# Kernel tuning notes

Hardware: AMD Instinct MI355X
Metric: run time of the kernel (lower is better)

## Reference

```python
import jax, jax.numpy as jnp
import numpy as np

NEG_SLOPE = 0.2   # PyG GATConv default negative_slope
LN_EPS = 1e-5
SOFTMAX_EPS = 1e-16  # PyG softmax denominator eps


def setup_inputs() -> dict:
    key = jax.random.key(0)
    ks = jax.random.split(key, 6)
    N, IN, OUT, H, E = 100000, 128, 64, 2, 1600000
    X = jax.random.normal(ks[0], (N, IN), dtype=jnp.float32)
    edge_index = jax.random.randint(ks[1], (2, E), 0, N, dtype=jnp.int64)
    W = jax.random.normal(ks[2], (H * OUT, IN), dtype=jnp.float32) * 0.05
    att_src = jax.random.normal(ks[3], (H, OUT), dtype=jnp.float32) * 0.05
    att_dst = jax.random.normal(ks[4], (H, OUT), dtype=jnp.float32) * 0.05
    bias = jnp.zeros((OUT,), dtype=jnp.float32)
    ln_gamma = jnp.ones((OUT,), dtype=jnp.float32)
    ln_beta = jnp.zeros((OUT,), dtype=jnp.float32)
    return {"X": X, "edge_index": edge_index, "W": W, "att_src": att_src,
            "att_dst": att_dst, "bias": bias, "ln_gamma": ln_gamma, "ln_beta": ln_beta}


def reference(X, edge_index, W, att_src, att_dst, bias, ln_gamma, ln_beta):
    N = X.shape[0]
    H, F = att_src.shape
    # PyG GATConv default: add self-loops
    loops = jnp.arange(N, dtype=edge_index.dtype)
    src = jnp.concatenate([edge_index[0], loops])  # [Et]
    dst = jnp.concatenate([edge_index[1], loops])  # [Et]
    # linear projection: x' = X @ W^T  -> [N, H, F]
    x = (X @ W.T).reshape(N, H, F)
    # per-node attention logits  [N, H]
    a_src = jnp.einsum('nhf,hf->nh', x, att_src)
    a_dst = jnp.einsum('nhf,hf->nh', x, att_dst)
    # per-edge logits, leaky relu  [Et, H]
    e = jax.nn.leaky_relu(a_src[src] + a_dst[dst], NEG_SLOPE)
    # segment softmax over incoming edges of each dst node
    m = jax.ops.segment_max(e, dst, num_segments=N)          # [N, H]
    ex = jnp.exp(e - m[dst])
    denom = jax.ops.segment_sum(ex, dst, num_segments=N)     # [N, H]
    alpha = ex / (denom[dst] + SOFTMAX_EPS)                  # [Et, H]
    # weighted scatter-add of source features
    msg = x[src] * alpha[:, :, None]                         # [Et, H, F]
    out = jax.ops.segment_sum(msg, dst, num_segments=N)      # [N, H, F]
    # concat=False -> mean over heads, then bias
    out = out.mean(axis=1) + bias                            # [N, F]
    # LayerNorm over features
    mu = out.mean(axis=-1, keepdims=True)
    var = ((out - mu) ** 2).mean(axis=-1, keepdims=True)
    h = (out - mu) * jax.lax.rsqrt(var + LN_EPS) * ln_gamma + ln_beta
    return h
```

## Files before the change

kernel.cpp:

```cpp
#include <hip/hip_runtime.h>
#include <hip/hip_bf16.h>

#define NEG_SLOPE 0.2f
#define LN_EPS 1e-5f
#define SM_EPS 1e-16f

typedef __attribute__((ext_vector_type(8))) short bf16x8;
typedef __attribute__((ext_vector_type(4))) float f32x4;

__device__ inline unsigned short f2bf(float f) {
    unsigned u = __float_as_uint(f);
    return (unsigned short)((u + 0x7FFFu + ((u >> 16) & 1u)) >> 16);
}
__device__ inline float bf_lo(unsigned int v) { return __uint_as_float(v << 16); }
__device__ inline float bf_hi(unsigned int v) { return __uint_as_float(v & 0xffff0000u); }

#define NBIN 512
#define BCAP 4864
#define SCHUNK 4096
#define CURPAD 16

__global__ __launch_bounds__(256) void k_gemm(const float* __restrict__ X,
                                              const float* __restrict__ W,
                                              const float* __restrict__ att_src,
                                              const float* __restrict__ att_dst,
                                              unsigned int* __restrict__ xp,
                                              float2* __restrict__ aS,
                                              float2* __restrict__ aD,
                                              int* __restrict__ binCursor, int N) {
    __shared__ unsigned short Ws[128 * 136];
    __shared__ unsigned short Xs[64 * 136];
    const int t = threadIdx.x;
    const int b0 = blockIdx.x * 64;
    const int lane = t & 63;
    const int w = t >> 6;
    const int c15 = lane & 15;
    const int quad = lane >> 4;

    if (blockIdx.x == 0) {
        for (int i = t; i < NBIN; i += 256) binCursor[i * CURPAD] = i * BCAP;
    }

#pragma unroll
    for (int i = 0; i < 16; ++i) {
        int f = i * 256 + t;
        int nr = f >> 5;
        int q = f & 31;
        float4 v = reinterpret_cast<const float4*>(W)[nr * 32 + q];
        ushort4 b;
        b.x = f2bf(v.x); b.y = f2bf(v.y); b.z = f2bf(v.z); b.w = f2bf(v.w);
        *reinterpret_cast<ushort4*>(&Ws[nr * 136 + q * 4]) = b;
    }
#pragma unroll
    for (int i = 0; i < 8; ++i) {
        int f = i * 256 + t;
        int m = f >> 5;
        int q = f & 31;
        int gr = b0 + m;
        if (gr >= N) gr = N - 1;
        float4 v = reinterpret_cast<const float4*>(X)[(size_t)gr * 32 + q];
        ushort4 b;
        b.x = f2bf(v.x); b.y = f2bf(v.y); b.z = f2bf(v.z); b.w = f2bf(v.w);
        *reinterpret_cast<ushort4*>(&Xs[m * 136 + q * 4]) = b;
    }
    __syncthreads();

    f32x4 acc[8];
#pragma unroll
    for (int ct = 0; ct < 8; ++ct) acc[ct] = (f32x4){0.f, 0.f, 0.f, 0.f};

#pragma unroll
    for (int kc = 0; kc < 4; ++kc) {
        bf16x8 af = *reinterpret_cast<const bf16x8*>(
            &Xs[(w * 16 + c15) * 136 + kc * 32 + quad * 8]);
#pragma unroll
        for (int ct = 0; ct < 8; ++ct) {
            bf16x8 bfr = *reinterpret_cast<const bf16x8*>(
                &Ws[(ct * 16 + c15) * 136 + kc * 32 + quad * 8]);
            acc[ct] = __builtin_amdgcn_mfma_f32_16x16x32_bf16(af, bfr, acc[ct], 0, 0, 0);
        }
    }

    float attS[8], attD[8];
#pragma unroll
    for (int ct = 0; ct < 8; ++ct) {
        attS[ct] = att_src[ct * 16 + c15];
        attD[ct] = att_dst[ct * 16 + c15];
    }

#pragma unroll
    for (int r = 0; r < 4; ++r) {
        int row = b0 + w * 16 + quad * 4 + r;
        float s0 = 0.f, s1 = 0.f, d0 = 0.f, d1 = 0.f;
#pragma unroll
        for (int ct = 0; ct < 4; ++ct) {
            s0 += acc[ct][r] * attS[ct];
            d0 += acc[ct][r] * attD[ct];
            s1 += acc[ct + 4][r] * attS[ct + 4];
            d1 += acc[ct + 4][r] * attD[ct + 4];
        }
#pragma unroll
        for (int o = 1; o < 16; o <<= 1) {
            s0 += __shfl_xor(s0, o);
            s1 += __shfl_xor(s1, o);
            d0 += __shfl_xor(d0, o);
            d1 += __shfl_xor(d1, o);
        }
        if (row < N) {
#pragma unroll
            for (int ct = 0; ct < 4; ++ct) {
                unsigned int p = (unsigned int)f2bf(acc[ct][r]) |
                                 ((unsigned int)f2bf(acc[ct + 4][r]) << 16);
                xp[(size_t)row * 64 + ct * 16 + c15] = p;
            }
            if (c15 == 0) {
                aS[row] = make_float2(s0, s1);
                aD[row] = make_float2(d0, d1);
            }
        }
    }
}

__global__ __launch_bounds__(256) void k_scatter(const int* __restrict__ ei,
                                                 int* __restrict__ binCursor,
                                                 unsigned int* __restrict__ tmp,
                                                 int E) {
    __shared__ int off[NBIN];
    const int t = threadIdx.x;
    const int base = blockIdx.x * SCHUNK;

    int bn[16];
    unsigned int pe[16];
#pragma unroll
    for (int k = 0; k < 16; ++k) {
        int i = base + k * 256 + t;
        if (i < E) {
            int s = ei[i];
            int d = ei[E + i];
            bn[k] = d >> 8;
            pe[k] = ((unsigned)(d & 255) << 24) | (unsigned)s;
        } else {
            bn[k] = -1;
        }
    }

    for (int i = t; i < NBIN; i += 256) off[i] = 0;
    __syncthreads();
#pragma unroll
    for (int k = 0; k < 16; ++k)
        if (bn[k] >= 0) atomicAdd(&off[bn[k]], 1);
    __syncthreads();
    for (int i = t; i < NBIN; i += 256) {
        int h = off[i];
        off[i] = h ? atomicAdd(&binCursor[i * CURPAD], h) : 0;
    }
    __syncthreads();
#pragma unroll
    for (int k = 0; k < 16; ++k) {
        if (bn[k] >= 0) {
            int p = atomicAdd(&off[bn[k]], 1);
            tmp[p] = pe[k];
        }
    }
}

__global__ __launch_bounds__(512) void k_bucket(const unsigned int* __restrict__ tmp,
                                                const int* __restrict__ binCursor,
                                                unsigned int* __restrict__ csr,
                                                unsigned int* __restrict__ rowPtr,
                                                int N) {
    __shared__ int cnt[256];
    __shared__ int cur[256];
    __shared__ int lds[4];
    const int t = threadIdx.x;
    const int b = blockIdx.x;
    const int start = b * BCAP;
    int m = binCursor[b * CURPAD] - start;
    if (m > BCAP) m = BCAP;

    if (t < 256) cnt[t] = 0;
    __syncthreads();

    for (int k = t; k < m; k += 512) {
        atomicAdd(&cnt[tmp[start + k] >> 24], 1);
    }
    __syncthreads();

    const int lane = t & 63, w = t >> 6;
    int v = 0, incl = 0;
    if (t < 256) {
        v = cnt[t];
        incl = v;
#pragma unroll
        for (int o = 1; o < 64; o <<= 1) {
            int u = __shfl_up(incl, o);
            if (lane >= o) incl += u;
        }
        if (lane == 63) lds[w] = incl;
    }
    __syncthreads();
    if (t == 0) {
        int run = 0;
        for (int i = 0; i < 4; ++i) { int tv = lds[i]; lds[i] = run; run += tv; }
    }
    __syncthreads();
    if (t < 256) {
        int excl = lds[w] + incl - v;
        cur[t] = excl;
        int d = b * 256 + t;
        if (d < N) rowPtr[d] = (unsigned)(start + excl) | ((unsigned)v << 22);
    }
    __syncthreads();

    for (int k = t; k < m; k += 512) {
        unsigned int e = tmp[start + k];
        int p = atomicAdd(&cur[e >> 24], 1);
        csr[start + p] = e & 0x00FFFFFFu;
    }
}

__global__ __launch_bounds__(256) void k_agg(const unsigned int* __restrict__ xp,
                                             const float2* __restrict__ aS,
                                             const float2* __restrict__ aD,
                                             const unsigned int* __restrict__ rowPtr,
                                             const unsigned int* __restrict__ csr,
                                             const float* __restrict__ bias,
                                             const float* __restrict__ gamma,
                                             const float* __restrict__ beta,
                                             float* __restrict__ out, int N) {
    const int w = threadIdx.x >> 6, lane = threadIdx.x & 63;
    const int n = blockIdx.x * 4 + w;
    if (n >= N) return;

    float2 a = aS[n];
    float2 ad2 = aD[n];
    float f0 = a.x + ad2.x; f0 = fmaxf(f0, NEG_SLOPE * f0);
    float f1 = a.y + ad2.y; f1 = fmaxf(f1, NEG_SLOPE * f1);
    float us0 = __expf(f0), us1 = __expf(f1);

    unsigned int vself = xp[((unsigned)n << 6) | lane];
    float S0 = us0 * bf_lo(vself);
    float S1 = us1 * bf_hi(vself);
    float D0 = us0, D1 = us1;

    unsigned int pr = rowPtr[n];
    const int jb = (int)(pr & 0x3FFFFFu);
    const int je = jb + (int)(pr >> 22);
    int j = jb;
    const int nfull = (je - jb) >> 3;

    unsigned int cc[8];
    if (nfull > 0) {
        int ju = __builtin_amdgcn_readfirstlane(j);
#pragma unroll
        for (int q = 0; q < 8; ++q) cc[q] = csr[ju + q];
    }
    for (int bI = 0; bI < nfull; ++bI) {
        unsigned int v[8];
        float2 as_[8];
#pragma unroll
        for (int q = 0; q < 8; ++q) v[q] = xp[(cc[q] << 6) | lane];
#pragma unroll
        for (int q = 0; q < 8; ++q) as_[q] = aS[cc[q]];
        unsigned int cn[8];
        {
            int jn = (bI + 1 < nfull) ? (j + 8) : jb;
            int ju = __builtin_amdgcn_readfirstlane(jn);
#pragma unroll
            for (int q = 0; q < 8; ++q) cn[q] = csr[ju + q];
        }
#pragma unroll
        for (int q = 0; q < 8; ++q) {
            float g0 = as_[q].x + ad2.x; g0 = fmaxf(g0, NEG_SLOPE * g0);
            float g1 = as_[q].y + ad2.y; g1 = fmaxf(g1, NEG_SLOPE * g1);
            float u0 = __expf(g0), u1 = __expf(g1);
            D0 += u0; D1 += u1;
            S0 += u0 * bf_lo(v[q]);
            S1 += u1 * bf_hi(v[q]);
        }
#pragma unroll
        for (int q = 0; q < 8; ++q) cc[q] = cn[q];
        j += 8;
    }
    for (; j + 3 < je; j += 4) {
        int ju = __builtin_amdgcn_readfirstlane(j);
        unsigned int c[4];
#pragma unroll
        for (int q = 0; q < 4; ++q) c[q] = csr[ju + q];
        unsigned int v[4];
        float2 as_[4];
#pragma unroll
        for (int q = 0; q < 4; ++q) v[q] = xp[(c[q] << 6) | lane];
#pragma unroll
        for (int q = 0; q < 4; ++q) as_[q] = aS[c[q]];
#pragma unroll
        for (int q = 0; q < 4; ++q) {
            float g0 = as_[q].x + ad2.x; g0 = fmaxf(g0, NEG_SLOPE * g0);
            float g1 = as_[q].y + ad2.y; g1 = fmaxf(g1, NEG_SLOPE * g1);
            float u0 = __expf(g0), u1 = __expf(g1);
            D0 += u0; D1 += u1;
            S0 += u0 * bf_lo(v[q]);
            S1 += u1 * bf_hi(v[q]);
        }
    }
    for (; j < je; ++j) {
        unsigned int c = csr[__builtin_amdgcn_readfirstlane(j)];
        unsigned int vv = xp[(c << 6) | lane];
        float2 asv = aS[c];
        float g0 = asv.x + ad2.x; g0 = fmaxf(g0, NEG_SLOPE * g0);
        float g1 = asv.y + ad2.y; g1 = fmaxf(g1, NEG_SLOPE * g1);
        float u0 = __expf(g0), u1 = __expf(g1);
        D0 += u0; D1 += u1;
        S0 += u0 * bf_lo(vv);
        S1 += u1 * bf_hi(vv);
    }

    float o = (0.5f / (D0 + SM_EPS)) * S0 + (0.5f / (D1 + SM_EPS)) * S1 + bias[lane];

    float mu = o;
#pragma unroll
    for (int d = 32; d > 0; d >>= 1) mu += __shfl_xor(mu, d);
    mu *= (1.0f / 64.0f);
    float dv = o - mu;
    float var = dv * dv;
#pragma unroll
    for (int d = 32; d > 0; d >>= 1) var += __shfl_xor(var, d);
    var *= (1.0f / 64.0f);
    out[(size_t)n * 64 + lane] = dv * rsqrtf(var + LN_EPS) * gamma[lane] + beta[lane];
}

extern "C" void kernel_launch(void* const* d_in, const int* in_sizes, int n_in,
                              void* d_out, int out_size, void* d_ws, size_t ws_size,
                              hipStream_t stream) {
    const float* X        = (const float*)d_in[0];
    const int*   ei       = (const int*)d_in[1];
    const float* W        = (const float*)d_in[2];
    const float* att_src  = (const float*)d_in[3];
    const float* att_dst  = (const float*)d_in[4];
    const float* bias     = (const float*)d_in[5];
    const float* ln_gamma = (const float*)d_in[6];
    const float* ln_beta  = (const float*)d_in[7];
    float* out = (float*)d_out;

    const int N = in_sizes[0] / 128;
    const int E = in_sizes[1] / 2;
    const int NBUCK = (N + 255) / 256;

    char* ws = (char*)d_ws;
    size_t off = 0;
    auto alloc = [&](size_t bytes) {
        size_t o = off;
        off += (bytes + 255) & ~(size_t)255;
        return o;
    };
    unsigned int* xp     = (unsigned int*)(ws + alloc((size_t)N * 64 * 4));
    float2* aS           = (float2*)(ws + alloc((size_t)N * 8));
    float2* aD           = (float2*)(ws + alloc((size_t)N * 8));
    unsigned int* rowPtr = (unsigned int*)(ws + alloc((size_t)N * 4));
    unsigned int* csr    = (unsigned int*)(ws + alloc((size_t)NBIN * BCAP * 4));
    unsigned int* tmp    = (unsigned int*)(ws + alloc((size_t)NBIN * BCAP * 4));
    int* binCursor       = (int*)(ws + alloc(NBIN * CURPAD * 4));

    k_gemm<<<(N + 63) / 64, 256, 0, stream>>>(X, W, att_src, att_dst, xp, aS, aD,
                                              binCursor, N);
    k_scatter<<<(E + SCHUNK - 1) / SCHUNK, 256, 0, stream>>>(ei, binCursor, tmp, E);
    k_bucket<<<NBUCK, 512, 0, stream>>>(tmp, binCursor, csr, rowPtr, N);
    k_agg<<<(N + 3) / 4, 256, 0, stream>>>(xp, aS, aD, rowPtr, csr,
                                           bias, ln_gamma, ln_beta, out, N);
}
```

Measured before the change: 231.2 us.

## Fuse bucketing and aggregation into one kernel with per-edge exp precomputed in LDS

Bins are narrowed to 64 destinations each (2048 bins), and the separate bucket-sort and aggregation kernels are merged into one fused kernel. Each block loads its bin's edges, computes the attention exp weights once per edge (packed as bf16), accumulates softmax denominators with LDS atomics, sorts the edges locally in LDS, and then each wave aggregates 16 destination nodes from LDS. This drops the csr/rowPtr global round trip and a kernel launch, and computes each edge's exp once. In exchange the softmax weights are stored in bf16, there is no max-subtraction, bin capacity is tight (1344 per 64 nodes, against an average of about 1024) so overflow edges would be silently dropped, and the cursor reset now uses an extra memset.

```diff
diff --git a/kernel.cpp b/kernel.cpp
--- a/kernel.cpp
+++ b/kernel.cpp
@@ -15,8 +15,9 @@
 __device__ inline float bf_lo(unsigned int v) { return __uint_as_float(v << 16); }
 __device__ inline float bf_hi(unsigned int v) { return __uint_as_float(v & 0xffff0000u); }
 
-#define NBIN 512
-#define BCAP 4864
+#define NBIN2 2048
+#define BCAP2 1344
+#define DPB 64
 #define SCHUNK 4096
 #define CURPAD 16
 
@@ -26,8 +27,7 @@
                                               const float* __restrict__ att_dst,
                                               unsigned int* __restrict__ xp,
                                               float2* __restrict__ aS,
-                                              float2* __restrict__ aD,
-                                              int* __restrict__ binCursor, int N) {
+                                              float2* __restrict__ aD, int N) {
     __shared__ unsigned short Ws[128 * 136];
     __shared__ unsigned short Xs[64 * 136];
     const int t = threadIdx.x;
@@ -36,10 +36,6 @@
     const int w = t >> 6;
     const int c15 = lane & 15;
     const int quad = lane >> 4;
-
-    if (blockIdx.x == 0) {
-        for (int i = t; i < NBIN; i += 256) binCursor[i * CURPAD] = i * BCAP;
-    }
 
 #pragma unroll
     for (int i = 0; i < 16; ++i) {
@@ -125,7 +121,7 @@
                                                  int* __restrict__ binCursor,
                                                  unsigned int* __restrict__ tmp,
                                                  int E) {
-    __shared__ int off[NBIN];
+    __shared__ int off[NBIN2];
     const int t = threadIdx.x;
     const int base = blockIdx.x * SCHUNK;
 
@@ -137,22 +133,22 @@
         if (i < E) {
             int s = ei[i];
             int d = ei[E + i];
-            bn[k] = d >> 8;
-            pe[k] = ((unsigned)(d & 255) << 24) | (unsigned)s;
+            bn[k] = d >> 6;
+            pe[k] = ((unsigned)(d & 63) << 26) | (unsigned)s;
         } else {
             bn[k] = -1;
         }
     }
 
-    for (int i = t; i < NBIN; i += 256) off[i] = 0;
+    for (int i = t; i < NBIN2; i += 256) off[i] = 0;
     __syncthreads();
 #pragma unroll
     for (int k = 0; k < 16; ++k)
         if (bn[k] >= 0) atomicAdd(&off[bn[k]], 1);
     __syncthreads();
-    for (int i = t; i < NBIN; i += 256) {
+    for (int i = t; i < NBIN2; i += 256) {
         int h = off[i];
-        off[i] = h ? atomicAdd(&binCursor[i * CURPAD], h) : 0;
+        off[i] = h ? (atomicAdd(&binCursor[i * CURPAD], h) + i * BCAP2) : 0;
     }
     __syncthreads();
 #pragma unroll
@@ -164,169 +160,142 @@
     }
 }
 
-__global__ __launch_bounds__(512) void k_bucket(const unsigned int* __restrict__ tmp,
-                                                const int* __restrict__ binCursor,
-                                                unsigned int* __restrict__ csr,
-                                                unsigned int* __restrict__ rowPtr,
-                                                int N) {
-    __shared__ int cnt[256];
-    __shared__ int cur[256];
-    __shared__ int lds[4];
+__global__ __launch_bounds__(256) void k_fused(const unsigned int* __restrict__ xp,
+                                               const float2* __restrict__ aS,
+                                               const float2* __restrict__ aD,
+                                               const unsigned int* __restrict__ tmp,
+                                               const int* __restrict__ binCursor,
+                                               const float* __restrict__ bias,
+                                               const float* __restrict__ gamma,
+                                               const float* __restrict__ beta,
+                                               float* __restrict__ out, int N) {
+    __shared__ int cnt[DPB];
+    __shared__ int cur[DPB];
+    __shared__ int beg[DPB];
+    __shared__ float den0[DPB], den1[DPB];
+    __shared__ float2 adc[DPB];
+    __shared__ uint2 ebuf[BCAP2];
     const int t = threadIdx.x;
     const int b = blockIdx.x;
-    const int start = b * BCAP;
-    int m = binCursor[b * CURPAD] - start;
-    if (m > BCAP) m = BCAP;
-
-    if (t < 256) cnt[t] = 0;
-    __syncthreads();
-
-    for (int k = t; k < m; k += 512) {
-        atomicAdd(&cnt[tmp[start + k] >> 24], 1);
-    }
-    __syncthreads();
-
-    const int lane = t & 63, w = t >> 6;
-    int v = 0, incl = 0;
-    if (t < 256) {
-        v = cnt[t];
-        incl = v;
+    const int start = b * BCAP2;
+    const int d0 = b * DPB;
+    int m = binCursor[b * CURPAD];
+    if (m > BCAP2) m = BCAP2;
+
+    if (t < DPB) {
+        cnt[t] = 0; den0[t] = 0.f; den1[t] = 0.f;
+        int d = d0 + t;
+        adc[t] = (d < N) ? aD[d] : make_float2(0.f, 0.f);
+    }
+    __syncthreads();
+
+    unsigned int ee[6], uu[6];
+#pragma unroll
+    for (int it = 0; it < 6; ++it) {
+        int k = t + it * 256;
+        ee[it] = 0xFFFFFFFFu;
+        if (k < m) {
+            unsigned int e = tmp[start + k];
+            ee[it] = e;
+            int li = e >> 26;
+            int s = (int)(e & 0x03FFFFFFu);
+            float2 as2 = aS[s];
+            float2 ad2 = adc[li];
+            float g0 = as2.x + ad2.x; g0 = fmaxf(g0, NEG_SLOPE * g0);
+            float g1 = as2.y + ad2.y; g1 = fmaxf(g1, NEG_SLOPE * g1);
+            unsigned int u01 = (unsigned)f2bf(__expf(g0)) |
+                               ((unsigned)f2bf(__expf(g1)) << 16);
+            uu[it] = u01;
+            atomicAdd(&cnt[li], 1);
+            atomicAdd(&den0[li], bf_lo(u01));
+            atomicAdd(&den1[li], bf_hi(u01));
+        }
+    }
+    __syncthreads();
+
+    if (t < DPB) {
+        int v = cnt[t];
+        int incl = v;
 #pragma unroll
         for (int o = 1; o < 64; o <<= 1) {
             int u = __shfl_up(incl, o);
-            if (lane >= o) incl += u;
-        }
-        if (lane == 63) lds[w] = incl;
-    }
-    __syncthreads();
-    if (t == 0) {
-        int run = 0;
-        for (int i = 0; i < 4; ++i) { int tv = lds[i]; lds[i] = run; run += tv; }
-    }
-    __syncthreads();
-    if (t < 256) {
-        int excl = lds[w] + incl - v;
-        cur[t] = excl;
-        int d = b * 256 + t;
-        if (d < N) rowPtr[d] = (unsigned)(start + excl) | ((unsigned)v << 22);
-    }
-    __syncthreads();
-
-    for (int k = t; k < m; k += 512) {
-        unsigned int e = tmp[start + k];
-        int p = atomicAdd(&cur[e >> 24], 1);
-        csr[start + p] = e & 0x00FFFFFFu;
-    }
-}
-
-__global__ __launch_bounds__(256) void k_agg(const unsigned int* __restrict__ xp,
-                                             const float2* __restrict__ aS,
-                                             const float2* __restrict__ aD,
-                                             const unsigned int* __restrict__ rowPtr,
-                                             const unsigned int* __restrict__ csr,
-                                             const float* __restrict__ bias,
-                                             const float* __restrict__ gamma,
-                                             const float* __restrict__ beta,
-                                             float* __restrict__ out, int N) {
-    const int w = threadIdx.x >> 6, lane = threadIdx.x & 63;
-    const int n = blockIdx.x * 4 + w;
-    if (n >= N) return;
-
-    float2 a = aS[n];
-    float2 ad2 = aD[n];
-    float f0 = a.x + ad2.x; f0 = fmaxf(f0, NEG_SLOPE * f0);
-    float f1 = a.y + ad2.y; f1 = fmaxf(f1, NEG_SLOPE * f1);
-    float us0 = __expf(f0), us1 = __expf(f1);
-
-    unsigned int vself = xp[((unsigned)n << 6) | lane];
-    float S0 = us0 * bf_lo(vself);
-    float S1 = us1 * bf_hi(vself);
-    float D0 = us0, D1 = us1;
-
-    unsigned int pr = rowPtr[n];
-    const int jb = (int)(pr & 0x3FFFFFu);
-    const int je = jb + (int)(pr >> 22);
-    int j = jb;
-    const int nfull = (je - jb) >> 3;
-
-    unsigned int cc[8];
-    if (nfull > 0) {
-        int ju = __builtin_amdgcn_readfirstlane(j);
-#pragma unroll
-        for (int q = 0; q < 8; ++q) cc[q] = csr[ju + q];
-    }
-    for (int bI = 0; bI < nfull; ++bI) {
-        unsigned int v[8];
-        float2 as_[8];
-#pragma unroll
-        for (int q = 0; q < 8; ++q) v[q] = xp[(cc[q] << 6) | lane];
-#pragma unroll
-        for (int q = 0; q < 8; ++q) as_[q] = aS[cc[q]];
-        unsigned int cn[8];
-        {
-            int jn = (bI + 1 < nfull) ? (j + 8) : jb;
-            int ju = __builtin_amdgcn_readfirstlane(jn);
-#pragma unroll
-            for (int q = 0; q < 8; ++q) cn[q] = csr[ju + q];
-        }
-#pragma unroll
-        for (int q = 0; q < 8; ++q) {
-            float g0 = as_[q].x + ad2.x; g0 = fmaxf(g0, NEG_SLOPE * g0);
-            float g1 = as_[q].y + ad2.y; g1 = fmaxf(g1, NEG_SLOPE * g1);
-            float u0 = __expf(g0), u1 = __expf(g1);
-            D0 += u0; D1 += u1;
-            S0 += u0 * bf_lo(v[q]);
-            S1 += u1 * bf_hi(v[q]);
-        }
-#pragma unroll
-        for (int q = 0; q < 8; ++q) cc[q] = cn[q];
-        j += 8;
-    }
-    for (; j + 3 < je; j += 4) {
-        int ju = __builtin_amdgcn_readfirstlane(j);
-        unsigned int c[4];
-#pragma unroll
-        for (int q = 0; q < 4; ++q) c[q] = csr[ju + q];
-        unsigned int v[4];
-        float2 as_[4];
-#pragma unroll
-        for (int q = 0; q < 4; ++q) v[q] = xp[(c[q] << 6) | lane];
-#pragma unroll
-        for (int q = 0; q < 4; ++q) as_[q] = aS[c[q]];
-#pragma unroll
-        for (int q = 0; q < 4; ++q) {
-            float g0 = as_[q].x + ad2.x; g0 = fmaxf(g0, NEG_SLOPE * g0);
-            float g1 = as_[q].y + ad2.y; g1 = fmaxf(g1, NEG_SLOPE * g1);
-            float u0 = __expf(g0), u1 = __expf(g1);
-            D0 += u0; D1 += u1;
-            S0 += u0 * bf_lo(v[q]);
-            S1 += u1 * bf_hi(v[q]);
-        }
-    }
-    for (; j < je; ++j) {
-        unsigned int c = csr[__builtin_amdgcn_readfirstlane(j)];
-        unsigned int vv = xp[(c << 6) | lane];
-        float2 asv = aS[c];
-        float g0 = asv.x + ad2.x; g0 = fmaxf(g0, NEG_SLOPE * g0);
-        float g1 = asv.y + ad2.y; g1 = fmaxf(g1, NEG_SLOPE * g1);
-        float u0 = __expf(g0), u1 = __expf(g1);
-        D0 += u0; D1 += u1;
-        S0 += u0 * bf_lo(vv);
-        S1 += u1 * bf_hi(vv);
-    }
-
-    float o = (0.5f / (D0 + SM_EPS)) * S0 + (0.5f / (D1 + SM_EPS)) * S1 + bias[lane];
-
-    float mu = o;
-#pragma unroll
-    for (int d = 32; d > 0; d >>= 1) mu += __shfl_xor(mu, d);
-    mu *= (1.0f / 64.0f);
-    float dv = o - mu;
-    float var = dv * dv;
-#pragma unroll
-    for (int d = 32; d > 0; d >>= 1) var += __shfl_xor(var, d);
-    var *= (1.0f / 64.0f);
-    out[(size_t)n * 64 + lane] = dv * rsqrtf(var + LN_EPS) * gamma[lane] + beta[lane];
+            if (t >= o) incl += u;
+        }
+        beg[t] = incl - v;
+        cur[t] = incl - v;
+    }
+    __syncthreads();
+
+#pragma unroll
+    for (int it = 0; it < 6; ++it) {
+        if (ee[it] != 0xFFFFFFFFu) {
+            int li = ee[it] >> 26;
+            int p = atomicAdd(&cur[li], 1);
+            ebuf[p] = make_uint2(ee[it] & 0x03FFFFFFu, uu[it]);
+        }
+    }
+    __syncthreads();
+
+    const int w = t >> 6, lane = t & 63;
+    for (int dd = 0; dd < 16; ++dd) {
+        int li = w * 16 + dd;
+        int n = d0 + li;
+        if (n >= N) break;
+
+        float2 a = aS[n];
+        float2 ad2 = adc[li];
+        float f0 = a.x + ad2.x; f0 = fmaxf(f0, NEG_SLOPE * f0);
+        float f1 = a.y + ad2.y; f1 = fmaxf(f1, NEG_SLOPE * f1);
+        float us0 = __expf(f0), us1 = __expf(f1);
+
+        unsigned int vself = xp[((unsigned)n << 6) | lane];
+        float S0 = us0 * bf_lo(vself);
+        float S1 = us1 * bf_hi(vself);
+        float inv0 = 0.5f / (den0[li] + us0 + SM_EPS);
+        float inv1 = 0.5f / (den1[li] + us1 + SM_EPS);
+
+        const int jb = beg[li];
+        const int je = jb + cnt[li];
+        int j = jb;
+        for (; j + 3 < je; j += 4) {
+            uint2 c0 = ebuf[j];
+            uint2 c1 = ebuf[j + 1];
+            uint2 c2 = ebuf[j + 2];
+            uint2 c3 = ebuf[j + 3];
+            unsigned int v0 = xp[(c0.x << 6) | lane];
+            unsigned int v1 = xp[(c1.x << 6) | lane];
+            unsigned int v2 = xp[(c2.x << 6) | lane];
+            unsigned int v3 = xp[(c3.x << 6) | lane];
+            S0 = fmaf(bf_lo(c0.y), bf_lo(v0), S0);
+            S1 = fmaf(bf_hi(c0.y), bf_hi(v0), S1);
+            S0 = fmaf(bf_lo(c1.y), bf_lo(v1), S0);
+            S1 = fmaf(bf_hi(c1.y), bf_hi(v1), S1);
+            S0 = fmaf(bf_lo(c2.y), bf_lo(v2), S0);
+            S1 = fmaf(bf_hi(c2.y), bf_hi(v2), S1);
+            S0 = fmaf(bf_lo(c3.y), bf_lo(v3), S0);
+            S1 = fmaf(bf_hi(c3.y), bf_hi(v3), S1);
+        }
+        for (; j < je; ++j) {
+            uint2 c = ebuf[j];
+            unsigned int vv = xp[(c.x << 6) | lane];
+            S0 = fmaf(bf_lo(c.y), bf_lo(vv), S0);
+            S1 = fmaf(bf_hi(c.y), bf_hi(vv), S1);
+        }
+
+        float o = inv0 * S0 + inv1 * S1 + bias[lane];
+
+        float mu = o;
+#pragma unroll
+        for (int d = 32; d > 0; d >>= 1) mu += __shfl_xor(mu, d);
+        mu *= (1.0f / 64.0f);
+        float dv = o - mu;
+        float var = dv * dv;
+#pragma unroll
+        for (int d = 32; d > 0; d >>= 1) var += __shfl_xor(var, d);
+        var *= (1.0f / 64.0f);
+        out[(size_t)n * 64 + lane] =
+            dv * rsqrtf(var + LN_EPS) * gamma[lane] + beta[lane];
+    }
 }
 
 extern "C" void kernel_launch(void* const* d_in, const int* in_sizes, int n_in,
@@ -344,7 +313,7 @@
 
     const int N = in_sizes[0] / 128;
     const int E = in_sizes[1] / 2;
-    const int NBUCK = (N + 255) / 256;
+    const int NB = (N + DPB - 1) / DPB;
 
     char* ws = (char*)d_ws;
     size_t off = 0;
@@ -356,15 +325,12 @@
     unsigned int* xp     = (unsigned int*)(ws + alloc((size_t)N * 64 * 4));
     float2* aS           = (float2*)(ws + alloc((size_t)N * 8));
     float2* aD           = (float2*)(ws + alloc((size_t)N * 8));
-    unsigned int* rowPtr = (unsigned int*)(ws + alloc((size_t)N * 4));
-    unsigned int* csr    = (unsigned int*)(ws + alloc((size_t)NBIN * BCAP * 4));
-    unsigned int* tmp    = (unsigned int*)(ws + alloc((size_t)NBIN * BCAP * 4));
-    int* binCursor       = (int*)(ws + alloc(NBIN * CURPAD * 4));
-
-    k_gemm<<<(N + 63) / 64, 256, 0, stream>>>(X, W, att_src, att_dst, xp, aS, aD,
-                                              binCursor, N);
+    unsigned int* tmp    = (unsigned int*)(ws + alloc((size_t)NBIN2 * BCAP2 * 4));
+    int* binCursor       = (int*)(ws + alloc((size_t)NBIN2 * CURPAD * 4));
+
+    hipMemsetAsync(binCursor, 0, (size_t)NBIN2 * CURPAD * 4, stream);
+    k_gemm<<<(N + 63) / 64, 256, 0, stream>>>(X, W, att_src, att_dst, xp, aS, aD, N);
     k_scatter<<<(E + SCHUNK - 1) / SCHUNK, 256, 0, stream>>>(ei, binCursor, tmp, E);
-    k_bucket<<<NBUCK, 512, 0, stream>>>(tmp, binCursor, csr, rowPtr, N);
-    k_agg<<<(N + 3) / 4, 256, 0, stream>>>(xp, aS, aD, rowPtr, csr,
-                                           bias, ln_gamma, ln_beta, out, N);
-}
+    k_fused<<<NB, 256, 0, stream>>>(xp, aS, aD, tmp, binCursor,
+                                    bias, ln_gamma, ln_beta, out, N);
+}
```

After: 251.0 us. 1.09x slower.
